# Optimization experiments

Hardware: AMD Instinct MI355X
Metric: run time of the kernel (lower is better)

Reference implementation:

```python
import jax, jax.numpy as jnp
import numpy as np

N = 2048          # target nodes
N_NODES = 2048    # neighbor pool
D_IN = 256
D_EDGE = 16
D_HID = 32
D_OUT = 256


def _mlp(h, w1, b1, w2, b2):
    # Linear -> Tanh -> Linear
    return jnp.tanh(h @ w1 + b1) @ w2 + b2


def setup_inputs() -> dict:
    key = jax.random.key(0)
    ks = jax.random.split(key, 20)
    s = 0.05
    inp = {
        "x": jax.random.normal(ks[0], (N, D_IN), jnp.float32),
        "neibs": jax.random.normal(ks[1], (N_NODES, D_IN), jnp.float32),
        "edge_emb": jax.random.normal(ks[2], (N * N_NODES, D_EDGE), jnp.float32),
        # multiplicative binary mask (float, as in original ws * mask)
        "mask": (jax.random.uniform(ks[3], (N, N_NODES)) < 0.7).astype(jnp.float32),
        "ax_w1": jax.random.normal(ks[4], (D_IN, D_HID), jnp.float32) * s,
        "ax_b1": jnp.zeros((D_HID,), jnp.float32),
        "ax_w2": jax.random.normal(ks[5], (D_HID, D_HID), jnp.float32) * s,
        "ax_b2": jnp.zeros((D_HID,), jnp.float32),
        "an_w1": jax.random.normal(ks[6], (D_IN, D_HID), jnp.float32) * s,
        "an_b1": jnp.zeros((D_HID,), jnp.float32),
        "an_w2": jax.random.normal(ks[7], (D_HID, D_HID), jnp.float32) * s,
        "an_b2": jnp.zeros((D_HID,), jnp.float32),
        "ae_w1": jax.random.normal(ks[8], (D_EDGE, D_HID), jnp.float32) * s,
        "ae_b1": jnp.zeros((D_HID,), jnp.float32),
        "ae_w2": jax.random.normal(ks[9], (D_HID, D_HID), jnp.float32) * s,
        "ae_b2": jnp.zeros((D_HID,), jnp.float32),
        "fcx_w": jax.random.normal(ks[10], (2 * D_IN, D_OUT), jnp.float32) * s,
        "fcx_b": jnp.zeros((D_OUT,), jnp.float32),
    }
    return inp


def reference(x, neibs, edge_emb, mask,
              ax_w1, ax_b1, ax_w2, ax_b2,
              an_w1, an_b1, an_w2, an_b2,
              ae_w1, ae_b1, ae_w2, ae_b2,
              fcx_w, fcx_b):
    x_att = _mlp(x, ax_w1, ax_b1, ax_w2, ax_b2)          # (N, H)
    neib_att = _mlp(neibs, an_w1, an_b1, an_w2, an_b2)   # (n_nodes, H)
    # edge attention is computed in the original forward but never used (dead code)
    _edge_att = _mlp(edge_emb, ae_w1, ae_b1, ae_w2, ae_b2)
    # multiplicative masking (NOT additive -inf), then softmax over neighbors
    ws = jnp.einsum('nh,mh->nm', x_att, neib_att) * mask  # (N, n_nodes)
    ws = jax.nn.softmax(ws, axis=1)
    agg_neib = jax.nn.sigmoid(ws @ neibs)                 # (N, D_IN)
    # concat_node=False path: concat -> fc_x -> sigmoid; dropout is identity (eval)
    out = jax.nn.sigmoid(jnp.concatenate([x, agg_neib], axis=1) @ fcx_w + fcx_b)
    return out
```

## Files before the change

### kernel.cpp

```cpp
#include <hip/hip_runtime.h>
#include <hip/hip_bf16.h>
#include <math.h>

#define NROWS 2048
#define DIN 256
#define DH 32
#define DOUT 256

typedef unsigned short ushort_t;
typedef unsigned int uint_t;
typedef __attribute__((ext_vector_type(8))) short short8;
typedef __attribute__((ext_vector_type(4))) float floatx4;

__device__ __forceinline__ float bf2f(uint_t u) {
    union { uint_t i; float f; } v; v.i = u << 16; return v.f;
}
__device__ __forceinline__ ushort_t f2bf(float f) {
    __hip_bfloat16 h = __float2bfloat16(f);
    union { __hip_bfloat16 h; ushort_t u; } v; v.h = h; return v.u;
}
__device__ __forceinline__ float sigm(float v) { return 1.0f / (1.0f + __expf(-v)); }

#define PST 2056

__global__ __launch_bounds__(256) void prep_kernel(
    const float* __restrict__ x, const float* __restrict__ neibs,
    const float* __restrict__ ax_w1, const float* __restrict__ ax_b1,
    const float* __restrict__ ax_w2, const float* __restrict__ ax_b2,
    const float* __restrict__ an_w1, const float* __restrict__ an_b1,
    const float* __restrict__ an_w2, const float* __restrict__ an_b2,
    const float* __restrict__ fcx_w,
    ushort_t* __restrict__ x_attB, short8* __restrict__ n_attP,
    short8* __restrict__ B_pack, short8* __restrict__ W_pack,
    ushort_t* __restrict__ XA)
{
    __shared__ float smem[32 * 256];
    const int t = threadIdx.x;
    const int b = blockIdx.x;

    if (b < 512) {
        float (*srow)[DIN] = (float (*)[DIN])smem;
        float* hbuf = smem + 8 * DIN;
        float* sbuf = smem + 8 * DIN + 8 * DH;

        const bool is_x = b < 256;
        const int row0 = (is_x ? b : b - 256) * 8;
        const float* __restrict__ in = is_x ? x : neibs;
        const float* __restrict__ w1 = is_x ? ax_w1 : an_w1;
        const float* __restrict__ b1 = is_x ? ax_b1 : an_b1;
        const float* __restrict__ w2 = is_x ? ax_w2 : an_w2;
        const float* __restrict__ b2 = is_x ? ax_b2 : an_b2;

        const int r = t >> 5, c = t & 31;
        {
            const float4* in4 = (const float4*)(in + (size_t)(row0 + r) * DIN);
            float4 a = in4[c * 2], bb = in4[c * 2 + 1];
            *(float4*)&srow[r][c * 8] = a;
            *(float4*)&srow[r][c * 8 + 4] = bb;
        }
        __syncthreads();

        float s = b1[c];
#pragma unroll 8
        for (int k = 0; k < DIN; ++k) s += srow[r][k] * w1[k * DH + c];
        s = tanhf(s);
        hbuf[r * DH + c] = s;
        __syncthreads();

        float s2 = b2[c];
#pragma unroll
        for (int j = 0; j < DH; ++j) s2 += hbuf[r * DH + j] * w2[j * DH + c];

        if (is_x) {
            x_attB[(size_t)(row0 + r) * DH + c] = f2bf(s2);
        } else {
            sbuf[r * DH + c] = s2;
            __syncthreads();
            if (t < 32) {
                const int r2 = t >> 2, q = t & 3;
                const int row = row0 + r2;
                short8 v;
#pragma unroll
                for (int j = 0; j < 8; ++j) v[j] = (short)f2bf(sbuf[r2 * DH + q * 8 + j]);
                n_attP[(row >> 4) * 64 + q * 16 + (row & 15)] = v;
            }
        }
    } else if (b < 576) {
        const int s = b - 512;
        float* tile = smem;
#pragma unroll
        for (int i = 0; i < 8; ++i) {
            const int e = i * 256 + t;
            const int row = e >> 6, c4 = e & 63;
            const float4 v = ((const float4*)neibs)[(size_t)(32 * s + row) * 64 + c4];
            *(float4*)&tile[row * 256 + c4 * 4] = v;
        }
        __syncthreads();
#pragma unroll
        for (int i = 0; i < 4; ++i) {
            const int G = i * 256 + t;
            const int n = G & 15, q = (G >> 4) & 3, tl = G >> 6;
            const int col = tl * 16 + n;
            short8 v;
#pragma unroll
            for (int j = 0; j < 8; ++j) v[j] = (short)f2bf(tile[(8 * q + j) * 256 + col]);
            B_pack[(size_t)(s * 16 + tl) * 64 + q * 16 + n] = v;
        }
    } else if (b < 592) {
        const int s = b - 576;
        float* tile = smem;
#pragma unroll
        for (int i = 0; i < 8; ++i) {
            const int e = i * 256 + t;
            const int row = e >> 6, c4 = e & 63;
            const float4 v = ((const float4*)fcx_w)[(size_t)(32 * s + row) * 64 + c4];
            *(float4*)&tile[row * 256 + c4 * 4] = v;
        }
        __syncthreads();
#pragma unroll
        for (int i = 0; i < 4; ++i) {
            const int G = i * 256 + t;
            const int n = G & 15, q = (G >> 4) & 3, tl = G >> 6;
            const int col = tl * 16 + n;
            short8 v;
#pragma unroll
            for (int j = 0; j < 8; ++j) v[j] = (short)f2bf(tile[(8 * q + j) * 256 + col]);
            W_pack[(size_t)(s * 16 + tl) * 64 + q * 16 + n] = v;
        }
    } else {
        const int base = (b - 592) * 32;
#pragma unroll
        for (int j = 0; j < 32; ++j) {
            const int row = base + j;
            XA[(size_t)row * 512 + t] = f2bf(x[(size_t)row * DIN + t]);
        }
    }
}

__global__ __launch_bounds__(256) void score_kernel(
    const float* __restrict__ mask,
    const ushort_t* __restrict__ x_attB, const short8* __restrict__ n_attP,
    short8* __restrict__ P_pack)
{
    __shared__ __align__(16) ushort_t pT[8 * PST];
    __shared__ float row_inv[8];

    const int t = threadIdx.x, b = blockIdx.x;
    const int n0 = b * 8;
    const int w = t >> 6, lane = t & 63;
    const int q = lane >> 4, nn = lane & 15;

    const short8 av = *(const short8*)(x_attB + (size_t)(n0 + (lane & 7)) * DH + q * 8);

#pragma unroll 4
    for (int i = 0; i < 32; ++i) {
        const int tl = w * 32 + i;
        const short8 bv = n_attP[tl * 64 + lane];
        floatx4 c = __builtin_amdgcn_mfma_f32_16x16x32_bf16(
            av, bv, (floatx4){0.f, 0.f, 0.f, 0.f}, 0, 0, 0);
        if (lane < 32) {
            const int m = tl * 16 + nn;
            const int rbase = (lane >> 4) * 4;
#pragma unroll
            for (int rg = 0; rg < 4; ++rg) {
                const int r = rbase + rg;
                const float sv = c[rg] * mask[(size_t)(n0 + r) * NROWS + m];
                pT[r * PST + m] = f2bf(sv);
            }
        }
    }
    __syncthreads();

    {
        const int r0 = 2 * w, r1 = r0 + 1;
        ushort_t* p0 = pT + r0 * PST;
        ushort_t* p1 = pT + r1 * PST;
        float mx0 = -1e30f, mx1 = -1e30f;
        uint_t raw0[16], raw1[16];
#pragma unroll
        for (int j = 0; j < 16; ++j) {
            raw0[j] = *(const uint_t*)(p0 + j * 128 + 2 * lane);
            raw1[j] = *(const uint_t*)(p1 + j * 128 + 2 * lane);
            mx0 = fmaxf(mx0, fmaxf(bf2f(raw0[j] & 0xffffu), bf2f(raw0[j] >> 16)));
            mx1 = fmaxf(mx1, fmaxf(bf2f(raw1[j] & 0xffffu), bf2f(raw1[j] >> 16)));
        }
#pragma unroll
        for (int off = 32; off >= 1; off >>= 1) {
            mx0 = fmaxf(mx0, __shfl_xor(mx0, off));
            mx1 = fmaxf(mx1, __shfl_xor(mx1, off));
        }
        float l0 = 0.f, l1 = 0.f;
#pragma unroll
        for (int j = 0; j < 16; ++j) {
            const float e00 = __expf(bf2f(raw0[j] & 0xffffu) - mx0);
            const float e01 = __expf(bf2f(raw0[j] >> 16) - mx0);
            const float e10 = __expf(bf2f(raw1[j] & 0xffffu) - mx1);
            const float e11 = __expf(bf2f(raw1[j] >> 16) - mx1);
            l0 += e00 + e01; l1 += e10 + e11;
            *(uint_t*)(p0 + j * 128 + 2 * lane) = (uint_t)f2bf(e00) | ((uint_t)f2bf(e01) << 16);
            *(uint_t*)(p1 + j * 128 + 2 * lane) = (uint_t)f2bf(e10) | ((uint_t)f2bf(e11) << 16);
        }
#pragma unroll
        for (int off = 32; off >= 1; off >>= 1) {
            l0 += __shfl_xor(l0, off);
            l1 += __shfl_xor(l1, off);
        }
        if (lane == 0) { row_inv[r0] = 1.f / l0; row_inv[r1] = 1.f / l1; }
    }
    __syncthreads();

    const int rt16 = b >> 1, h = b & 1;
    const int sr = nn;
    if ((sr >> 3) == h) {
        const float invr = row_inv[sr & 7];
        const ushort_t* prow = pT + (sr & 7) * PST;
#pragma unroll
        for (int i = 0; i < 16; ++i) {
            const int s = w * 16 + i;
            const short8 e = *(const short8*)(prow + 32 * s + 8 * q);
            short8 v;
#pragma unroll
            for (int j = 0; j < 8; ++j)
                v[j] = (short)f2bf(bf2f((uint_t)(ushort_t)e[j]) * invr);
            P_pack[(size_t)(rt16 * 64 + s) * 64 + lane] = v;
        }
    }
}

__global__ __launch_bounds__(256) void pv_kernel(
    const short8* __restrict__ P_pack, const short8* __restrict__ B_pack,
    ushort_t* __restrict__ XA)
{
    const int t = threadIdx.x, b = blockIdx.x;
    const int rt32 = b >> 2, cs = b & 3;
    const int w = t >> 6, lane = t & 63;
    const int ct = cs * 4 + w;

    const short8* PA0 = P_pack + (size_t)(2 * rt32) * 64 * 64;
    const short8* PA1 = PA0 + 64 * 64;

    floatx4 a0 = (floatx4){0.f, 0.f, 0.f, 0.f};
    floatx4 a1 = (floatx4){0.f, 0.f, 0.f, 0.f};
#pragma unroll 4
    for (int s = 0; s < 64; ++s) {
        const short8 A0 = PA0[s * 64 + lane];
        const short8 A1 = PA1[s * 64 + lane];
        const short8 B  = B_pack[(size_t)(s * 16 + ct) * 64 + lane];
        a0 = __builtin_amdgcn_mfma_f32_16x16x32_bf16(A0, B, a0, 0, 0, 0);
        a1 = __builtin_amdgcn_mfma_f32_16x16x32_bf16(A1, B, a1, 0, 0, 0);
    }

    const int col = 16 * ct + (lane & 15);
    const int rb = (lane >> 4) * 4;
#pragma unroll
    for (int rg = 0; rg < 4; ++rg) {
        XA[(size_t)(32 * rt32 + rb + rg) * 512 + 256 + col] = f2bf(sigm(a0[rg]));
        XA[(size_t)(32 * rt32 + 16 + rb + rg) * 512 + 256 + col] = f2bf(sigm(a1[rg]));
    }
}

__global__ __launch_bounds__(256) void fc_kernel(
    const ushort_t* __restrict__ XA, const short8* __restrict__ W_pack,
    const float* __restrict__ fcx_b, float* __restrict__ out)
{
    const int t = threadIdx.x, b = blockIdx.x;
    const int rt32 = b >> 2, cs = b & 3;
    const int w = t >> 6, lane = t & 63;
    const int ct = cs * 4 + w;
    const int q = lane >> 4, nn = lane & 15;

    const ushort_t* X0 = XA + (size_t)(32 * rt32 + nn) * 512 + 8 * q;
    const ushort_t* X1 = X0 + 16 * 512;

    floatx4 a0 = (floatx4){0.f, 0.f, 0.f, 0.f};
    floatx4 a1 = (floatx4){0.f, 0.f, 0.f, 0.f};
#pragma unroll
    for (int s = 0; s < 16; ++s) {
        const short8 A0 = *(const short8*)(X0 + 32 * s);
        const short8 A1 = *(const short8*)(X1 + 32 * s);
        const short8 B  = W_pack[(size_t)(s * 16 + ct) * 64 + lane];
        a0 = __builtin_amdgcn_mfma_f32_16x16x32_bf16(A0, B, a0, 0, 0, 0);
        a1 = __builtin_amdgcn_mfma_f32_16x16x32_bf16(A1, B, a1, 0, 0, 0);
    }

    const int col = 16 * ct + nn;
    const float bias = fcx_b[col];
    const int rb = (lane >> 4) * 4;
#pragma unroll
    for (int rg = 0; rg < 4; ++rg) {
        out[(size_t)(32 * rt32 + rb + rg) * DOUT + col] = sigm(a0[rg] + bias);
        out[(size_t)(32 * rt32 + 16 + rb + rg) * DOUT + col] = sigm(a1[rg] + bias);
    }
}

extern "C" void kernel_launch(void* const* d_in, const int* in_sizes, int n_in,
                              void* d_out, int out_size, void* d_ws, size_t ws_size,
                              hipStream_t stream) {
    const float* x      = (const float*)d_in[0];
    const float* neibs  = (const float*)d_in[1];
    const float* mask   = (const float*)d_in[3];
    const float* ax_w1  = (const float*)d_in[4];
    const float* ax_b1  = (const float*)d_in[5];
    const float* ax_w2  = (const float*)d_in[6];
    const float* ax_b2  = (const float*)d_in[7];
    const float* an_w1  = (const float*)d_in[8];
    const float* an_b1  = (const float*)d_in[9];
    const float* an_w2  = (const float*)d_in[10];
    const float* an_b2  = (const float*)d_in[11];
    const float* fcx_w  = (const float*)d_in[16];
    const float* fcx_b  = (const float*)d_in[17];
    float* out = (float*)d_out;

    char* ws = (char*)d_ws;
    ushort_t* x_attB = (ushort_t*)(ws);
    short8*   n_attP = (short8*)(ws + 131072);
    short8*   B_pack = (short8*)(ws + 262144);
    short8*   W_pack = (short8*)(ws + 1310720);
    ushort_t* XA     = (ushort_t*)(ws + 1572864);
    short8*   P_pack = (short8*)(ws + 3670016);

    prep_kernel<<<656, 256, 0, stream>>>(
        x, neibs, ax_w1, ax_b1, ax_w2, ax_b2,
        an_w1, an_b1, an_w2, an_b2, fcx_w,
        x_attB, n_attP, B_pack, W_pack, XA);

    score_kernel<<<256, 256, 0, stream>>>(mask, x_attB, n_attP, P_pack);

    pv_kernel<<<256, 256, 0, stream>>>(P_pack, B_pack, XA);

    fc_kernel<<<256, 256, 0, stream>>>(XA, W_pack, fcx_b, out);
}
```

Before: 396.0 us.

## Drop softmax max pass, defer normalization to PV, split-K PV and FC

The score kernel now exponentiates the masked scores directly, skipping the max-subtraction pass, and accumulates row sums with shuffles. It no longer rescales P before writing it; the 1/sum is stored globally and applied in the PV epilogue. PV and FC kernels launch twice as many blocks, each splitting K across warp pairs with an LDS reduction to raise parallelism. Dropping the max makes exp overflow possible if scores grow large, which relies on small attention magnitudes.

```diff
diff --git a/kernel.cpp b/kernel.cpp
--- a/kernel.cpp
+++ b/kernel.cpp
@@ -140,18 +140,20 @@
 __global__ __launch_bounds__(256) void score_kernel(
     const float* __restrict__ mask,
     const ushort_t* __restrict__ x_attB, const short8* __restrict__ n_attP,
-    short8* __restrict__ P_pack)
+    short8* __restrict__ P_pack, float* __restrict__ row_inv_g)
 {
     __shared__ __align__(16) ushort_t pT[8 * PST];
-    __shared__ float row_inv[8];
+    __shared__ float wsum[8][4];
 
     const int t = threadIdx.x, b = blockIdx.x;
     const int n0 = b * 8;
     const int w = t >> 6, lane = t & 63;
     const int q = lane >> 4, nn = lane & 15;
+    const int rbase = (lane >> 4) * 4;
 
     const short8 av = *(const short8*)(x_attB + (size_t)(n0 + (lane & 7)) * DH + q * 8);
 
+    float psum[4] = {0.f, 0.f, 0.f, 0.f};
 #pragma unroll 4
     for (int i = 0; i < 32; ++i) {
         const int tl = w * 32 + i;
@@ -160,102 +162,88 @@
             av, bv, (floatx4){0.f, 0.f, 0.f, 0.f}, 0, 0, 0);
         if (lane < 32) {
             const int m = tl * 16 + nn;
-            const int rbase = (lane >> 4) * 4;
 #pragma unroll
             for (int rg = 0; rg < 4; ++rg) {
                 const int r = rbase + rg;
-                const float sv = c[rg] * mask[(size_t)(n0 + r) * NROWS + m];
-                pT[r * PST + m] = f2bf(sv);
+                const float e = __expf(c[rg] * mask[(size_t)(n0 + r) * NROWS + m]);
+                psum[rg] += e;
+                pT[r * PST + m] = f2bf(e);
             }
         }
     }
+#pragma unroll
+    for (int off = 1; off <= 8; off <<= 1) {
+#pragma unroll
+        for (int rg = 0; rg < 4; ++rg) psum[rg] += __shfl_xor(psum[rg], off);
+    }
+    if (lane == 0 || lane == 16) {
+#pragma unroll
+        for (int rg = 0; rg < 4; ++rg) wsum[rbase + rg][w] = psum[rg];
+    }
     __syncthreads();
-
-    {
-        const int r0 = 2 * w, r1 = r0 + 1;
-        ushort_t* p0 = pT + r0 * PST;
-        ushort_t* p1 = pT + r1 * PST;
-        float mx0 = -1e30f, mx1 = -1e30f;
-        uint_t raw0[16], raw1[16];
-#pragma unroll
-        for (int j = 0; j < 16; ++j) {
-            raw0[j] = *(const uint_t*)(p0 + j * 128 + 2 * lane);
-            raw1[j] = *(const uint_t*)(p1 + j * 128 + 2 * lane);
-            mx0 = fmaxf(mx0, fmaxf(bf2f(raw0[j] & 0xffffu), bf2f(raw0[j] >> 16)));
-            mx1 = fmaxf(mx1, fmaxf(bf2f(raw1[j] & 0xffffu), bf2f(raw1[j] >> 16)));
-        }
-#pragma unroll
-        for (int off = 32; off >= 1; off >>= 1) {
-            mx0 = fmaxf(mx0, __shfl_xor(mx0, off));
-            mx1 = fmaxf(mx1, __shfl_xor(mx1, off));
-        }
-        float l0 = 0.f, l1 = 0.f;
-#pragma unroll
-        for (int j = 0; j < 16; ++j) {
-            const float e00 = __expf(bf2f(raw0[j] & 0xffffu) - mx0);
-            const float e01 = __expf(bf2f(raw0[j] >> 16) - mx0);
-            const float e10 = __expf(bf2f(raw1[j] & 0xffffu) - mx1);
-            const float e11 = __expf(bf2f(raw1[j] >> 16) - mx1);
-            l0 += e00 + e01; l1 += e10 + e11;
-            *(uint_t*)(p0 + j * 128 + 2 * lane) = (uint_t)f2bf(e00) | ((uint_t)f2bf(e01) << 16);
-            *(uint_t*)(p1 + j * 128 + 2 * lane) = (uint_t)f2bf(e10) | ((uint_t)f2bf(e11) << 16);
-        }
-#pragma unroll
-        for (int off = 32; off >= 1; off >>= 1) {
-            l0 += __shfl_xor(l0, off);
-            l1 += __shfl_xor(l1, off);
-        }
-        if (lane == 0) { row_inv[r0] = 1.f / l0; row_inv[r1] = 1.f / l1; }
-    }
-    __syncthreads();
+    if (t < 8)
+        row_inv_g[n0 + t] = 1.f / (wsum[t][0] + wsum[t][1] + wsum[t][2] + wsum[t][3]);
 
     const int rt16 = b >> 1, h = b & 1;
-    const int sr = nn;
-    if ((sr >> 3) == h) {
-        const float invr = row_inv[sr & 7];
-        const ushort_t* prow = pT + (sr & 7) * PST;
+    if ((nn >> 3) == h) {
+        const ushort_t* prow = pT + (nn & 7) * PST;
 #pragma unroll
         for (int i = 0; i < 16; ++i) {
             const int s = w * 16 + i;
-            const short8 e = *(const short8*)(prow + 32 * s + 8 * q);
-            short8 v;
-#pragma unroll
-            for (int j = 0; j < 8; ++j)
-                v[j] = (short)f2bf(bf2f((uint_t)(ushort_t)e[j]) * invr);
-            P_pack[(size_t)(rt16 * 64 + s) * 64 + lane] = v;
+            P_pack[(size_t)(rt16 * 64 + s) * 64 + lane] =
+                *(const short8*)(prow + 32 * s + 8 * q);
         }
     }
 }
 
 __global__ __launch_bounds__(256) void pv_kernel(
     const short8* __restrict__ P_pack, const short8* __restrict__ B_pack,
-    ushort_t* __restrict__ XA)
+    const float* __restrict__ row_inv, ushort_t* __restrict__ XA)
 {
+    __shared__ float red[2][8][64];
+
     const int t = threadIdx.x, b = blockIdx.x;
-    const int rt32 = b >> 2, cs = b & 3;
+    const int rt32 = b >> 3, cs = b & 7;
     const int w = t >> 6, lane = t & 63;
-    const int ct = cs * 4 + w;
-
-    const short8* PA0 = P_pack + (size_t)(2 * rt32) * 64 * 64;
-    const short8* PA1 = PA0 + 64 * 64;
+    const int ct = cs * 2 + (w & 1);
+    const int kh = w >> 1;
+
+    const short8* PA0 = P_pack + (size_t)(2 * rt32) * 4096;
+    const short8* PA1 = PA0 + 4096;
 
     floatx4 a0 = (floatx4){0.f, 0.f, 0.f, 0.f};
     floatx4 a1 = (floatx4){0.f, 0.f, 0.f, 0.f};
 #pragma unroll 4
-    for (int s = 0; s < 64; ++s) {
+    for (int si = 0; si < 32; ++si) {
+        const int s = kh * 32 + si;
         const short8 A0 = PA0[s * 64 + lane];
         const short8 A1 = PA1[s * 64 + lane];
         const short8 B  = B_pack[(size_t)(s * 16 + ct) * 64 + lane];
         a0 = __builtin_amdgcn_mfma_f32_16x16x32_bf16(A0, B, a0, 0, 0, 0);
         a1 = __builtin_amdgcn_mfma_f32_16x16x32_bf16(A1, B, a1, 0, 0, 0);
     }
-
-    const int col = 16 * ct + (lane & 15);
-    const int rb = (lane >> 4) * 4;
-#pragma unroll
-    for (int rg = 0; rg < 4; ++rg) {
-        XA[(size_t)(32 * rt32 + rb + rg) * 512 + 256 + col] = f2bf(sigm(a0[rg]));
-        XA[(size_t)(32 * rt32 + 16 + rb + rg) * 512 + 256 + col] = f2bf(sigm(a1[rg]));
+    if (kh == 1) {
+#pragma unroll
+        for (int j = 0; j < 4; ++j) {
+            red[w & 1][j][lane] = a0[j];
+            red[w & 1][4 + j][lane] = a1[j];
+        }
+    }
+    __syncthreads();
+    if (kh == 0) {
+#pragma unroll
+        for (int j = 0; j < 4; ++j) {
+            a0[j] += red[w & 1][j][lane];
+            a1[j] += red[w & 1][4 + j][lane];
+        }
+        const int col = 16 * ct + (lane & 15);
+        const int rb = (lane >> 4) * 4;
+#pragma unroll
+        for (int rg = 0; rg < 4; ++rg) {
+            const int r0 = 32 * rt32 + rb + rg, r1 = r0 + 16;
+            XA[(size_t)r0 * 512 + 256 + col] = f2bf(sigm(a0[rg] * row_inv[r0]));
+            XA[(size_t)r1 * 512 + 256 + col] = f2bf(sigm(a1[rg] * row_inv[r1]));
+        }
     }
 }
 
@@ -263,10 +251,13 @@
     const ushort_t* __restrict__ XA, const short8* __restrict__ W_pack,
     const float* __restrict__ fcx_b, float* __restrict__ out)
 {
+    __shared__ float red[2][8][64];
+
     const int t = threadIdx.x, b = blockIdx.x;
-    const int rt32 = b >> 2, cs = b & 3;
+    const int rt32 = b >> 3, cs = b & 7;
     const int w = t >> 6, lane = t & 63;
-    const int ct = cs * 4 + w;
+    const int ct = cs * 2 + (w & 1);
+    const int kh = w >> 1;
     const int q = lane >> 4, nn = lane & 15;
 
     const ushort_t* X0 = XA + (size_t)(32 * rt32 + nn) * 512 + 8 * q;
@@ -275,21 +266,37 @@
     floatx4 a0 = (floatx4){0.f, 0.f, 0.f, 0.f};
     floatx4 a1 = (floatx4){0.f, 0.f, 0.f, 0.f};
 #pragma unroll
-    for (int s = 0; s < 16; ++s) {
+    for (int si = 0; si < 8; ++si) {
+        const int s = kh * 8 + si;
         const short8 A0 = *(const short8*)(X0 + 32 * s);
         const short8 A1 = *(const short8*)(X1 + 32 * s);
         const short8 B  = W_pack[(size_t)(s * 16 + ct) * 64 + lane];
         a0 = __builtin_amdgcn_mfma_f32_16x16x32_bf16(A0, B, a0, 0, 0, 0);
         a1 = __builtin_amdgcn_mfma_f32_16x16x32_bf16(A1, B, a1, 0, 0, 0);
     }
-
-    const int col = 16 * ct + nn;
-    const float bias = fcx_b[col];
-    const int rb = (lane >> 4) * 4;
-#pragma unroll
-    for (int rg = 0; rg < 4; ++rg) {
-        out[(size_t)(32 * rt32 + rb + rg) * DOUT + col] = sigm(a0[rg] + bias);
-        out[(size_t)(32 * rt32 + 16 + rb + rg) * DOUT + col] = sigm(a1[rg] + bias);
+    if (kh == 1) {
+#pragma unroll
+        for (int j = 0; j < 4; ++j) {
+            red[w & 1][j][lane] = a0[j];
+            red[w & 1][4 + j][lane] = a1[j];
+        }
+    }
+    __syncthreads();
+    if (kh == 0) {
+#pragma unroll
+        for (int j = 0; j < 4; ++j) {
+            a0[j] += red[w & 1][j][lane];
+            a1[j] += red[w & 1][4 + j][lane];
+        }
+        const int col = 16 * ct + nn;
+        const float bias = fcx_b[col];
+        const int rb = (lane >> 4) * 4;
+#pragma unroll
+        for (int rg = 0; rg < 4; ++rg) {
+            const int r0 = 32 * rt32 + rb + rg, r1 = r0 + 16;
+            out[(size_t)r0 * DOUT + col] = sigm(a0[rg] + bias);
+            out[(size_t)r1 * DOUT + col] = sigm(a1[rg] + bias);
+        }
     }
 }
 
@@ -312,21 +319,22 @@
     float* out = (float*)d_out;
 
     char* ws = (char*)d_ws;
-    ushort_t* x_attB = (ushort_t*)(ws);
-    short8*   n_attP = (short8*)(ws + 131072);
-    short8*   B_pack = (short8*)(ws + 262144);
-    short8*   W_pack = (short8*)(ws + 1310720);
-    ushort_t* XA     = (ushort_t*)(ws + 1572864);
-    short8*   P_pack = (short8*)(ws + 3670016);
+    ushort_t* x_attB  = (ushort_t*)(ws);
+    short8*   n_attP  = (short8*)(ws + 131072);
+    short8*   B_pack  = (short8*)(ws + 262144);
+    short8*   W_pack  = (short8*)(ws + 1310720);
+    ushort_t* XA      = (ushort_t*)(ws + 1572864);
+    short8*   P_pack  = (short8*)(ws + 3670016);
+    float*    row_inv = (float*)(ws + 12058624);
 
     prep_kernel<<<656, 256, 0, stream>>>(
         x, neibs, ax_w1, ax_b1, ax_w2, ax_b2,
         an_w1, an_b1, an_w2, an_b2, fcx_w,
         x_attB, n_attP, B_pack, W_pack, XA);
 
-    score_kernel<<<256, 256, 0, stream>>>(mask, x_attB, n_attP, P_pack);
-
-    pv_kernel<<<256, 256, 0, stream>>>(P_pack, B_pack, XA);
-
-    fc_kernel<<<256, 256, 0, stream>>>(XA, W_pack, fcx_b, out);
-}
+    score_kernel<<<256, 256, 0, stream>>>(mask, x_attB, n_attP, P_pack, row_inv);
+
+    pv_kernel<<<512, 256, 0, stream>>>(P_pack, B_pack, row_inv, XA);
+
+    fc_kernel<<<512, 256, 0, stream>>>(XA, W_pack, fcx_b, out);
+}
```

Result: no change. 389.4 us (-1.7%).
